# Kernel optimization log

Measured on AMD Instinct MI355X. Metric: run time of the kernel, lower is better.

The kernel has to match this reference:

```python
import jax, jax.numpy as jnp
import numpy as np
import math

B, S, D, H = 16, 1024, 768, 12
Dh = D // H  # 64


def setup_inputs() -> dict:
    key = jax.random.key(0)
    ks = jax.random.split(key, 9)
    scale = 1.0 / math.sqrt(D)
    X = jax.random.normal(ks[0], (B, S, D), dtype=jnp.float32)
    # Per-head Q/K/V projections stacked along head dim: [H, D, Dh]
    Wq = jax.random.normal(ks[1], (H, D, Dh), dtype=jnp.float32) * scale
    Wk = jax.random.normal(ks[2], (H, D, Dh), dtype=jnp.float32) * scale
    Wv = jax.random.normal(ks[3], (H, D, Dh), dtype=jnp.float32) * scale
    bq = jax.random.normal(ks[4], (H, Dh), dtype=jnp.float32) * scale
    bk = jax.random.normal(ks[5], (H, Dh), dtype=jnp.float32) * scale
    bv = jax.random.normal(ks[6], (H, Dh), dtype=jnp.float32) * scale
    Wo = jax.random.normal(ks[7], (D, D), dtype=jnp.float32) * scale
    bo = jax.random.normal(ks[8], (D,), dtype=jnp.float32) * scale
    return {"X": X, "Wq": Wq, "bq": bq, "Wk": Wk, "bk": bk,
            "Wv": Wv, "bv": bv, "Wo": Wo, "bo": bo}


def reference(X, Wq, bq, Wk, bk, Wv, bv, Wo, bo):
    # Batched multi-head QKV projections (equivalent to the per-head Linear loop).
    Q = jnp.einsum('bsd,hde->bhse', X, Wq) + bq[None, :, None, :]
    K = jnp.einsum('bsd,hde->bhse', X, Wk) + bk[None, :, None, :]
    V = jnp.einsum('bsd,hde->bhse', X, Wv) + bv[None, :, None, :]
    scores = jnp.einsum('bhse,bhte->bhst', Q, K) / jnp.sqrt(jnp.float32(Dh))
    A = jax.nn.softmax(scores, axis=-1)            # [B,H,S,S]
    O = jnp.einsum('bhst,bhte->bhse', A, V)        # [B,H,S,Dh]
    # Concat heads along feature dim (matches torch cat order: head 0 first).
    msa = jnp.transpose(O, (0, 2, 1, 3)).reshape(B, S, D)
    return msa @ Wo + bo
```

## Files before the change

kernel.cpp:

```cpp
#include <hip/hip_runtime.h>
#include <hip/hip_bf16.h>

#define BB 16
#define SS 1024
#define DD 768
#define HH 12
#define DH 64

typedef short short8 __attribute__((ext_vector_type(8)));
typedef float f32x4 __attribute__((ext_vector_type(4)));
typedef float f32x16 __attribute__((ext_vector_type(16)));
typedef unsigned int uv2 __attribute__((ext_vector_type(2)));

__device__ inline float b2f(unsigned short v) {
    union { unsigned int u; float f; } x; x.u = ((unsigned int)v) << 16; return x.f;
}
__device__ inline unsigned short f2b(float f) {
    unsigned int u = __float_as_uint(f);
    u += 0x7FFFu + ((u >> 16) & 1u);
    return (unsigned short)(u >> 16);
}
__device__ inline unsigned int pk2(float a, float b) {
    __hip_bfloat162 h = __float22bfloat162_rn(make_float2(a, b));
    return *(unsigned int*)&h;
}
__device__ __forceinline__ float fast_exp2(float x) {
#if __has_builtin(__builtin_amdgcn_exp2f)
    return __builtin_amdgcn_exp2f(x);
#else
    return exp2f(x);
#endif
}
__device__ inline void cvt8(unsigned short* dst, const float* src) {
    const float4 f0 = *(const float4*)src;
    const float4 f1 = *(const float4*)(src + 4);
    unsigned short t[8] = {f2b(f0.x), f2b(f0.y), f2b(f0.z), f2b(f0.w),
                           f2b(f1.x), f2b(f1.y), f2b(f1.z), f2b(f1.w)};
    *(uint4*)dst = *(const uint4*)t;
}
__device__ __forceinline__ void async16(const void* g, void* l) {
    __builtin_amdgcn_global_load_lds(
        (const __attribute__((address_space(1))) void*)g,
        (__attribute__((address_space(3))) void*)l, 16, 0, 0);
}

__global__ __launch_bounds__(256) void detect_kernel(const unsigned short* __restrict__ X,
                                                     int* __restrict__ flag) {
    __shared__ int s;
    if (threadIdx.x == 0) s = 0;
    __syncthreads();
    int c = 0;
    for (int i = threadIdx.x; i < 16384; i += 256) {
        unsigned short v = X[i];
        if ((v & 0x7FFFu) >= 0x7F80u) c = 1;
    }
    if (c) s = 1;
    __syncthreads();
    if (threadIdx.x == 0) flag[0] = s;
}

__global__ __launch_bounds__(256) void prep_all(
    const void* __restrict__ Xv,
    const void* __restrict__ Wqv, const void* __restrict__ bqv,
    const void* __restrict__ Wkv, const void* __restrict__ bkv,
    const void* __restrict__ Wvv, const void* __restrict__ bvv,
    const void* __restrict__ Wov, const void* __restrict__ bov,
    const int* __restrict__ flag,
    unsigned short* __restrict__ Xb, unsigned short* __restrict__ Wc,
    unsigned short* __restrict__ Wot, unsigned short* __restrict__ bc,
    float* __restrict__ bo32)
{
    __shared__ unsigned short Ls[64][72];
    const int dt = *flag;
    const int u = threadIdx.x;
    const int bx = blockIdx.x;

    if (bx < 6144) {
        size_t base = ((size_t)bx * 256 + u) * 8;
        if (dt) cvt8(Xb + base, (const float*)Xv + base);
        else    *(uint4*)(Xb + base) = *(const uint4*)((const unsigned short*)Xv + base);
        return;
    }
    if (bx < 6720) {
        const int idx = bx - 6144;
        const int kt = idx % 12;
        const int y  = idx / 12;
        const int rk = u >> 2;
        const int e0 = (u & 3) * 16;

        const void* src; size_t srcBase;
        unsigned short* dst; int drow;
        if (y < 36) {
            int z = y / 12, h = y % 12;
            src = (z == 0) ? Wqv : (z == 1) ? Wkv : Wvv;
            srcBase = ((size_t)h * DD + kt * 64 + rk) * DH;
            dst = Wc; drow = z * 768 + h * 64;
        } else {
            int nt = y - 36;
            src = Wov;
            srcBase = (size_t)(kt * 64 + rk) * DD + nt * 64;
            dst = Wot; drow = nt * 64;
        }
#pragma unroll
        for (int ii = 0; ii < 2; ++ii) {
            int e = e0 + ii * 8;
            if (dt) {
                const float* p = (const float*)src + srcBase + e;
                float4 a = *(const float4*)p, b = *(const float4*)(p + 4);
                float v[8] = {a.x, a.y, a.z, a.w, b.x, b.y, b.z, b.w};
#pragma unroll
                for (int j = 0; j < 8; ++j) Ls[e + j][rk] = f2b(v[j]);
            } else {
                union { uint4 v; unsigned short s[8]; } t;
                t.v = *(const uint4*)((const unsigned short*)src + srcBase + e);
#pragma unroll
                for (int j = 0; j < 8; ++j) Ls[e + j][rk] = t.s[j];
            }
        }
        __syncthreads();
        const int e = u >> 2, q = u & 3;
#pragma unroll
        for (int ii = 0; ii < 2; ++ii) {
            int kk = q * 16 + ii * 8;
            *(uint4*)(dst + (size_t)(drow + e) * DD + kt * 64 + kk) = *(const uint4*)(&Ls[e][kk]);
        }
        return;
    }
    for (int n = u; n < 2304; n += 256) {
        int z = n / 768, i = n % 768;
        const void* b = (z == 0) ? bqv : (z == 1) ? bkv : bvv;
        bc[n] = dt ? f2b(((const float*)b)[i]) : ((const unsigned short*)b)[i];
    }
    for (int n = u; n < 768; n += 256)
        bo32[n] = dt ? ((const float*)bov)[n] : b2f(((const unsigned short*)bov)[n]);
}

__global__ __launch_bounds__(256) void qkv_gemm(
    const unsigned short* __restrict__ Xb,
    const unsigned short* __restrict__ Wc,
    const unsigned short* __restrict__ bc,
    unsigned short* __restrict__ Qb, unsigned short* __restrict__ Kb,
    unsigned short* __restrict__ Vtb)
{
    __shared__ __align__(16) unsigned short lds[17408];
    unsigned short* As = lds;
    unsigned short* Bs = lds + 128 * 64;

    const int u = threadIdx.x;
    const int lane = u & 63, w = u >> 6;
    const int ln = lane & 15, quad = lane >> 4;
    const int wm = w & 1, wn = w >> 1;

    const int nt0 = blockIdx.x;
    const int m0  = blockIdx.y << 7;
    const int n0  = nt0 << 7;
    const int z   = nt0 / 6;
    const int hpair = (nt0 % 6) * 2;

    const int rA = w * 32 + (lane >> 3);
    const int c8 = (((lane & 7) ^ (lane >> 3)) * 8);

    f32x4 acc[4][4];
#pragma unroll
    for (int i = 0; i < 4; ++i)
#pragma unroll
        for (int j = 0; j < 4; ++j) acc[i][j] = (f32x4){0.f, 0.f, 0.f, 0.f};

    const unsigned short* Ag = Xb + (size_t)(m0 + rA) * DD + c8;
    const unsigned short* Bg = Wc + (size_t)(n0 + rA) * DD + c8;
    unsigned short* lA0 = As + w * 2048;
    unsigned short* lB0 = Bs + w * 2048;

    for (int kb = 0; kb < 12; ++kb) {
        const int k0 = kb * 64;
        if (kb) __syncthreads();
#pragma unroll
        for (int j = 0; j < 4; ++j) {
            async16(Ag + (size_t)j * 8 * DD + k0, lA0 + j * 512);
            async16(Bg + (size_t)j * 8 * DD + k0, lB0 + j * 512);
        }
        __syncthreads();
#pragma unroll
        for (int kh = 0; kh < 2; ++kh) {
            const int sx = ((kh * 4 + quad) ^ (ln & 7)) * 8;
            short8 af[4], bf[4];
#pragma unroll
            for (int t = 0; t < 4; ++t) {
                af[t] = *(const short8*)(As + (wm * 64 + t * 16 + ln) * 64 + sx);
                bf[t] = *(const short8*)(Bs + (wn * 64 + t * 16 + ln) * 64 + sx);
            }
#pragma unroll
            for (int mt = 0; mt < 4; ++mt)
#pragma unroll
                for (int nt = 0; nt < 4; ++nt)
                    acc[mt][nt] = __builtin_amdgcn_mfma_f32_16x16x32_bf16(af[mt], bf[nt], acc[mt][nt], 0, 0, 0);
        }
    }

    float bias[4];
#pragma unroll
    for (int nt = 0; nt < 4; ++nt) bias[nt] = b2f(bc[n0 + wn * 64 + nt * 16 + ln]);

    const int b = m0 >> 10;
    if (z < 2) {
        unsigned short* O = (z == 0) ? Qb : Kb;
        const float sc = (z == 0) ? 0.180336880111120f : 1.0f;
        const int h = hpair + wn;
        const int sb = (m0 & 1023) + wm * 64;
#pragma unroll
        for (int mt = 0; mt < 4; ++mt)
#pragma unroll
            for (int r = 0; r < 4; ++r) {
                int s = sb + mt * 16 + quad * 4 + r;
                size_t rowo = ((size_t)(b * HH + h) * SS + s) * DH;
#pragma unroll
                for (int nt = 0; nt < 4; ++nt)
                    O[rowo + nt * 16 + ln] = f2b((acc[mt][nt][r] + bias[nt]) * sc);
            }
    } else {
        __syncthreads();
#pragma unroll
        for (int mt = 0; mt < 4; ++mt)
#pragma unroll
            for (int nt = 0; nt < 4; ++nt)
#pragma unroll
                for (int r = 0; r < 4; ++r)
                    lds[(wn * 64 + nt * 16 + ln) * 136 + wm * 64 + mt * 16 + quad * 4 + r] =
                        f2b(acc[mt][nt][r] + bias[nt]);
        __syncthreads();
        const int cc = u >> 1, half = u & 1;
        const int h = hpair + (cc >> 6), e = cc & 63;
        const int sb = (m0 & 1023) + half * 64;
        unsigned short* dst = Vtb + ((size_t)(b * HH + h) * DH + e) * SS + sb;
        const unsigned short* srcp = lds + cc * 136 + half * 64;
#pragma unroll
        for (int i = 0; i < 8; ++i)
            *(uint4*)(dst + i * 8) = *(const uint4*)(srcp + i * 8);
    }
}

__global__ __launch_bounds__(256, 3) void attn_kernel(
    const unsigned short* __restrict__ Kb,
    const unsigned short* __restrict__ Vtb,
    unsigned short* __restrict__ Qb)
{
    __shared__ __align__(16) unsigned short QPs[8192];
    __shared__ __align__(16) unsigned short Ks[2][4096];
    __shared__ __align__(16) unsigned short Vs[2][4096];

    const int u = threadIdx.x;
    const int flat = (blockIdx.y << 3) | blockIdx.x;
    const int swz  = (flat & 7) * 192 + (flat >> 3);
    const int s0 = (swz & 7) << 7;
    const int bh = swz >> 3;

    const int lane = u & 63, w = u >> 6;
    const int l31 = lane & 31, hi = lane >> 5;
    const int r7 = l31 & 7;

    unsigned short* Qg = Qb + ((size_t)bh * SS + s0) * DH;
    const unsigned short* Kg = Kb + (size_t)bh * SS * DH;
    const unsigned short* Vg = Vtb + (size_t)bh * DH * SS;

    const int srow = lane >> 3;
    const int cg8  = ((lane & 7) ^ srow) * 8;

    const unsigned short* kp0 = Kg + (size_t)((w * 2 + 0) * 8 + srow) * DH + cg8;
    const unsigned short* kp1 = Kg + (size_t)((w * 2 + 1) * 8 + srow) * DH + cg8;
    const unsigned short* vp0 = Vg + (size_t)((w * 2 + 0) * 8 + srow) * SS + cg8;
    const unsigned short* vp1 = Vg + (size_t)((w * 2 + 1) * 8 + srow) * SS + cg8;

#pragma unroll
    for (int j = 0; j < 4; ++j) {
        const int r0 = (w * 4 + j) * 8 + srow;
        async16(Qg + (size_t)r0 * DH + cg8, QPs + (w * 4 + j) * 512);
    }
    async16(kp0, &Ks[0][(w * 2 + 0) * 512]);
    async16(kp1, &Ks[0][(w * 2 + 1) * 512]);
    async16(vp0, &Vs[0][(w * 2 + 0) * 512]);
    async16(vp1, &Vs[0][(w * 2 + 1) * 512]);
    kp0 += 64 * DH; kp1 += 64 * DH; vp0 += 64; vp1 += 64;
    __syncthreads();

    short8 qf[4];
    {
        const unsigned short* qrow = QPs + (w * 32 + l31) * 64;
#pragma unroll
        for (int ke = 0; ke < 4; ++ke)
            qf[ke] = *(const short8*)(qrow + (((ke * 2 + hi) ^ r7) * 8));
    }

    int off[4];
#pragma unroll
    for (int x = 0; x < 4; ++x) off[x] = l31 * 64 + (((x * 2 + hi) ^ r7) * 8);

    f32x16 oA, oB;
#pragma unroll
    for (int i = 0; i < 16; ++i) { oA[i] = 0.f; oB[i] = 0.f; }
    float lsum = 0.f;

    for (int kt = 0; kt < 16; ++kt) {
        const int cur = kt & 1;
        if (kt < 15) {
            unsigned short* lk = &Ks[cur ^ 1][(w * 2) * 512];
            unsigned short* lv = &Vs[cur ^ 1][(w * 2) * 512];
            async16(kp0, lk);
            async16(kp1, lk + 512);
            async16(vp0, lv);
            async16(vp1, lv + 512);
            kp0 += 64 * DH; kp1 += 64 * DH; vp0 += 64; vp1 += 64;
        }
        const unsigned short* kc = Ks[cur];
        const unsigned short* vc = Vs[cur];

        f32x16 sA, sB;
#pragma unroll
        for (int i = 0; i < 16; ++i) { sA[i] = 0.f; sB[i] = 0.f; }
        __builtin_amdgcn_s_setprio(1);
#pragma unroll
        for (int ke = 0; ke < 4; ++ke) {
            short8 kf0 = *(const short8*)(kc + off[ke]);
            short8 kf1 = *(const short8*)(kc + off[ke] + 2048);
            sA = __builtin_amdgcn_mfma_f32_32x32x16_bf16(kf0, qf[ke], sA, 0, 0, 0);
            sB = __builtin_amdgcn_mfma_f32_32x32x16_bf16(kf1, qf[ke], sB, 0, 0, 0);
        }
        __builtin_amdgcn_s_setprio(0);

        unsigned int W0[8], W1[8];
#pragma unroll
        for (int i = 0; i < 8; ++i) {
            float a0 = fast_exp2(sA[2 * i]), b0 = fast_exp2(sA[2 * i + 1]);
            float a1 = fast_exp2(sB[2 * i]), b1 = fast_exp2(sB[2 * i + 1]);
            lsum += (a0 + b0) + (a1 + b1);
            W0[i] = pk2(a0, b0);
            W1[i] = pk2(a1, b1);
        }

        __builtin_amdgcn_s_setprio(1);
#define PV_STEP(Wt, ks) {                                                              \
        union { unsigned int wv[4]; short8 s; } pu;                                    \
        { uv2 rr = __builtin_amdgcn_permlane32_swap(Wt[4 * ((ks) & 1) + 0],            \
                                                    Wt[4 * ((ks) & 1) + 2], false, false); \
          pu.wv[0] = rr.x; pu.wv[2] = rr.y; }                                          \
        { uv2 rr = __builtin_amdgcn_permlane32_swap(Wt[4 * ((ks) & 1) + 1],            \
                                                    Wt[4 * ((ks) & 1) + 3], false, false); \
          pu.wv[1] = rr.x; pu.wv[3] = rr.y; }                                          \
        short8 vf0 = *(const short8*)(vc + off[(ks)]);                                 \
        short8 vf1 = *(const short8*)(vc + off[(ks)] + 2048);                          \
        oA = __builtin_amdgcn_mfma_f32_32x32x16_bf16(vf0, pu.s, oA, 0, 0, 0);          \
        oB = __builtin_amdgcn_mfma_f32_32x32x16_bf16(vf1, pu.s, oB, 0, 0, 0); }
        PV_STEP(W0, 0)
        PV_STEP(W0, 1)
        PV_STEP(W1, 2)
        PV_STEP(W1, 3)
#undef PV_STEP
        __builtin_amdgcn_s_setprio(0);

        __syncthreads();
    }

    float oth = __shfl(lsum, lane ^ 32, 64);
    const float linv = 1.f / (lsum + oth);

    unsigned short* Ob = QPs + w * 2048;
#define OSTORE(oc, et) {                                                   \
        _Pragma("unroll")                                                  \
        for (int rg = 0; rg < 4; ++rg) {                                   \
            uv2 wv;                                                        \
            wv.x = pk2(oc[rg * 4 + 0] * linv, oc[rg * 4 + 1] * linv);      \
            wv.y = pk2(oc[rg * 4 + 2] * linv, oc[rg * 4 + 3] * linv);      \
            *(uv2*)(Ob + l31 * 64 + ((((et) * 4 + rg) ^ r7) * 8) + hi * 4) = wv; \
        } }
    OSTORE(oA, 0)
    OSTORE(oB, 1)
#undef OSTORE

    const int rr2 = lane >> 1, q16 = lane & 1, rs = rr2 & 7;
    const unsigned short* orow = QPs + w * 2048 + rr2 * 64;
    unsigned short* gout = Qg + (size_t)(w * 32 + rr2) * DH;
#pragma unroll
    for (int i = 0; i < 4; ++i) {
        const int g = q16 * 4 + i;
        *(uint4*)(gout + g * 8) = *(const uint4*)(orow + ((g ^ rs) * 8));
    }
}

__global__ __launch_bounds__(256) void oproj_gemm(
    const unsigned short* __restrict__ Ob,
    const unsigned short* __restrict__ Wot,
    const float* __restrict__ bo32,
    float* __restrict__ out)
{
    __shared__ __align__(16) unsigned short lds[128 * 128];
    unsigned short* As = lds;
    unsigned short* Bs = lds + 128 * 64;

    const int u = threadIdx.x;
    const int lane = u & 63, w = u >> 6;
    const int ln = lane & 15, quad = lane >> 4;
    const int wm = w & 1, wn = w >> 1;

    const int n0 = blockIdx.x << 7;
    const int m0 = blockIdx.y << 7;
    const int b = m0 >> 10, s0t = m0 & 1023;

    const int rA = w * 32 + (lane >> 3);
    const int c8 = (((lane & 7) ^ (lane >> 3)) * 8);

    f32x4 acc[4][4];
#pragma unroll
    for (int i = 0; i < 4; ++i)
#pragma unroll
        for (int j = 0; j < 4; ++j) acc[i][j] = (f32x4){0.f, 0.f, 0.f, 0.f};

    const unsigned short* Bg = Wot + (size_t)(n0 + rA) * DD + c8;
    unsigned short* lA0 = As + w * 2048;
    unsigned short* lB0 = Bs + w * 2048;

    for (int kb = 0; kb < 12; ++kb) {
        if (kb) __syncthreads();
        const unsigned short* Ag = Ob + ((size_t)(b * HH + kb) * SS + s0t + rA) * DH + c8;
#pragma unroll
        for (int j = 0; j < 4; ++j) {
            async16(Ag + (size_t)j * 8 * DH, lA0 + j * 512);
            async16(Bg + (size_t)j * 8 * DD + kb * 64, lB0 + j * 512);
        }
        __syncthreads();
#pragma unroll
        for (int kh = 0; kh < 2; ++kh) {
            const int sx = ((kh * 4 + quad) ^ (ln & 7)) * 8;
            short8 af[4], bf[4];
#pragma unroll
            for (int t = 0; t < 4; ++t) {
                af[t] = *(const short8*)(As + (wm * 64 + t * 16 + ln) * 64 + sx);
                bf[t] = *(const short8*)(Bs + (wn * 64 + t * 16 + ln) * 64 + sx);
            }
#pragma unroll
            for (int mt = 0; mt < 4; ++mt)
#pragma unroll
                for (int nt = 0; nt < 4; ++nt)
                    acc[mt][nt] = __builtin_amdgcn_mfma_f32_16x16x32_bf16(af[mt], bf[nt], acc[mt][nt], 0, 0, 0);
        }
    }

    float bias[4];
#pragma unroll
    for (int nt = 0; nt < 4; ++nt) bias[nt] = bo32[n0 + wn * 64 + nt * 16 + ln];
#pragma unroll
    for (int mt = 0; mt < 4; ++mt)
#pragma unroll
        for (int r = 0; r < 4; ++r) {
            int m = m0 + wm * 64 + mt * 16 + quad * 4 + r;
            float* orow = out + (size_t)m * DD + n0 + wn * 64;
#pragma unroll
            for (int nt = 0; nt < 4; ++nt)
                orow[nt * 16 + ln] = acc[mt][nt][r] + bias[nt];
        }
}

extern "C" void kernel_launch(void* const* d_in, const int* in_sizes, int n_in,
                              void* d_out, int out_size, void* d_ws, size_t ws_size,
                              hipStream_t stream)
{
    const void* X  = d_in[0];
    const void* Wq = d_in[1];
    const void* bq = d_in[2];
    const void* Wk = d_in[3];
    const void* bk = d_in[4];
    const void* Wv = d_in[5];
    const void* bv = d_in[6];
    const void* Wo = d_in[7];
    const void* bo = d_in[8];
    float* out = (float*)d_out;

    const size_t NE = (size_t)BB * HH * SS * DH;
    char* p = (char*)d_ws;
    int* flag = (int*)p;                 p += 256;
    unsigned short* Qb  = (unsigned short*)p;  p += NE * 2;
    unsigned short* Kb  = (unsigned short*)p;  p += NE * 2;
    unsigned short* Vtb = (unsigned short*)p;  p += NE * 2;
    unsigned short* Xb  = (unsigned short*)p;  p += (size_t)BB * SS * DD * 2;
    unsigned short* Wc  = (unsigned short*)p;  p += (size_t)3 * DD * DD * 2;
    unsigned short* Wot = (unsigned short*)p;  p += (size_t)DD * DD * 2;
    unsigned short* bcb = (unsigned short*)p;  p += 4608;
    float* bo32 = (float*)p;                   p += 3072;

    detect_kernel<<<1, 256, 0, stream>>>((const unsigned short*)X, flag);
    prep_all<<<6721, 256, 0, stream>>>(X, Wq, bq, Wk, bk, Wv, bv, Wo, bo, flag,
                                       Xb, Wc, Wot, bcb, bo32);
    qkv_gemm<<<dim3(18, 128), 256, 0, stream>>>(Xb, Wc, bcb, Qb, Kb, Vtb);
    attn_kernel<<<dim3(8, 192), 256, 0, stream>>>(Kb, Vtb, Qb);
    oproj_gemm<<<dim3(6, 128), 256, 0, stream>>>(Qb, Wot, bo32, out);
}
```

Before: 301.1 us.

## Alias Q staging onto K buffer and compute softmax row sums via MFMA

Drops the dedicated Q LDS buffer by staging Q and the output tile through the K double-buffer, with an extra barrier. This cuts LDS per block so the launch bound can rise from 3 to 4 blocks per CU. It also replaces the per-lane scalar exp-sum with an extra MFMA against a ones vector, so the denominator comes from the same bf16-rounded P used for the numerator. The cost is one more MFMA per PV step, 16 more accumulator registers under a tighter register budget (possible spills), and more synchronisation.

```diff
diff --git a/kernel.cpp b/kernel.cpp
--- a/kernel.cpp
+++ b/kernel.cpp
@@ -239,14 +239,14 @@
     }
 }
 
-__global__ __launch_bounds__(256, 3) void attn_kernel(
+__global__ __launch_bounds__(256, 4) void attn_kernel(
     const unsigned short* __restrict__ Kb,
     const unsigned short* __restrict__ Vtb,
     unsigned short* __restrict__ Qb)
 {
-    __shared__ __align__(16) unsigned short QPs[8192];
     __shared__ __align__(16) unsigned short Ks[2][4096];
     __shared__ __align__(16) unsigned short Vs[2][4096];
+    unsigned short* KsF = &Ks[0][0];
 
     const int u = threadIdx.x;
     const int flat = (blockIdx.y << 3) | blockIdx.x;
@@ -273,8 +273,19 @@
 #pragma unroll
     for (int j = 0; j < 4; ++j) {
         const int r0 = (w * 4 + j) * 8 + srow;
-        async16(Qg + (size_t)r0 * DH + cg8, QPs + (w * 4 + j) * 512);
-    }
+        async16(Qg + (size_t)r0 * DH + cg8, KsF + (w * 4 + j) * 512);
+    }
+    __syncthreads();
+
+    short8 qf[4];
+    {
+        const unsigned short* qrow = KsF + (w * 32 + l31) * 64;
+#pragma unroll
+        for (int ke = 0; ke < 4; ++ke)
+            qf[ke] = *(const short8*)(qrow + (((ke * 2 + hi) ^ r7) * 8));
+    }
+    __syncthreads();
+
     async16(kp0, &Ks[0][(w * 2 + 0) * 512]);
     async16(kp1, &Ks[0][(w * 2 + 1) * 512]);
     async16(vp0, &Vs[0][(w * 2 + 0) * 512]);
@@ -282,22 +293,17 @@
     kp0 += 64 * DH; kp1 += 64 * DH; vp0 += 64; vp1 += 64;
     __syncthreads();
 
-    short8 qf[4];
-    {
-        const unsigned short* qrow = QPs + (w * 32 + l31) * 64;
-#pragma unroll
-        for (int ke = 0; ke < 4; ++ke)
-            qf[ke] = *(const short8*)(qrow + (((ke * 2 + hi) ^ r7) * 8));
-    }
+    short8 ones;
+#pragma unroll
+    for (int i = 0; i < 8; ++i) ones[i] = (short)0x3F80;
 
     int off[4];
 #pragma unroll
     for (int x = 0; x < 4; ++x) off[x] = l31 * 64 + (((x * 2 + hi) ^ r7) * 8);
 
-    f32x16 oA, oB;
-#pragma unroll
-    for (int i = 0; i < 16; ++i) { oA[i] = 0.f; oB[i] = 0.f; }
-    float lsum = 0.f;
+    f32x16 oA, oB, oL;
+#pragma unroll
+    for (int i = 0; i < 16; ++i) { oA[i] = 0.f; oB[i] = 0.f; oL[i] = 0.f; }
 
     for (int kt = 0; kt < 16; ++kt) {
         const int cur = kt & 1;
@@ -329,11 +335,8 @@
         unsigned int W0[8], W1[8];
 #pragma unroll
         for (int i = 0; i < 8; ++i) {
-            float a0 = fast_exp2(sA[2 * i]), b0 = fast_exp2(sA[2 * i + 1]);
-            float a1 = fast_exp2(sB[2 * i]), b1 = fast_exp2(sB[2 * i + 1]);
-            lsum += (a0 + b0) + (a1 + b1);
-            W0[i] = pk2(a0, b0);
-            W1[i] = pk2(a1, b1);
+            W0[i] = pk2(fast_exp2(sA[2 * i]), fast_exp2(sA[2 * i + 1]));
+            W1[i] = pk2(fast_exp2(sB[2 * i]), fast_exp2(sB[2 * i + 1]));
         }
 
         __builtin_amdgcn_s_setprio(1);
@@ -345,6 +348,7 @@
         { uv2 rr = __builtin_amdgcn_permlane32_swap(Wt[4 * ((ks) & 1) + 1],            \
                                                     Wt[4 * ((ks) & 1) + 3], false, false); \
           pu.wv[1] = rr.x; pu.wv[3] = rr.y; }                                          \
+        oL = __builtin_amdgcn_mfma_f32_32x32x16_bf16(ones, pu.s, oL, 0, 0, 0);         \
         short8 vf0 = *(const short8*)(vc + off[(ks)]);                                 \
         short8 vf1 = *(const short8*)(vc + off[(ks)] + 2048);                          \
         oA = __builtin_amdgcn_mfma_f32_32x32x16_bf16(vf0, pu.s, oA, 0, 0, 0);          \
@@ -359,10 +363,9 @@
         __syncthreads();
     }
 
-    float oth = __shfl(lsum, lane ^ 32, 64);
-    const float linv = 1.f / (lsum + oth);
-
-    unsigned short* Ob = QPs + w * 2048;
+    const float linv = 1.f / oL[0];
+
+    unsigned short* Ob = KsF + w * 2048;
 #define OSTORE(oc, et) {                                                   \
         _Pragma("unroll")                                                  \
         for (int rg = 0; rg < 4; ++rg) {                                   \
@@ -376,7 +379,7 @@
 #undef OSTORE
 
     const int rr2 = lane >> 1, q16 = lane & 1, rs = rr2 & 7;
-    const unsigned short* orow = QPs + w * 2048 + rr2 * 64;
+    const unsigned short* orow = KsF + w * 2048 + rr2 * 64;
     unsigned short* gout = Qg + (size_t)(w * 32 + rr2) * DH;
 #pragma unroll
     for (int i = 0; i < 4; ++i) {
```

Result: faster. 288.6 us (-4.2%).
